# Performance work log

Hardware: AMD Instinct MI355X
Metric: run time of the kernel (lower is better)

The kernel has to match this reference:

```python
import jax, jax.numpy as jnp
import numpy as np

D_MODEL = 256
D_STATE = 32
D_CONV = 8
EXPAND = 4
D_INNER = EXPAND * D_MODEL  # 1024
DT_RANK = (D_MODEL + 15) // 16  # 16
EPS = 1e-5


def setup_inputs() -> dict:
    key = jax.random.key(0)
    ks = jax.random.split(key, 12)
    s = lambda *sh: 1.0 / np.sqrt(sh[-1])
    inp = {
        "x": jax.random.normal(ks[0], (8, 1024, D_MODEL), dtype=jnp.float32),
        "norm_w": jnp.ones((D_MODEL,), jnp.float32),
        "norm_b": jnp.zeros((D_MODEL,), jnp.float32),
        "in_proj_w": jax.random.normal(ks[1], (2 * D_INNER, D_MODEL), jnp.float32) * s(D_MODEL),
        "conv_w": jax.random.normal(ks[2], (D_INNER, 1, D_CONV), jnp.float32) * s(D_CONV),
        "conv_b": jax.random.normal(ks[3], (D_INNER,), jnp.float32) * 0.02,
        "x_proj_w": jax.random.normal(ks[4], (DT_RANK + 2 * D_STATE, D_INNER), jnp.float32) * s(D_INNER),
        "dt_proj_w": jax.random.normal(ks[5], (D_INNER, DT_RANK), jnp.float32) * s(DT_RANK),
        "dt_proj_b": jax.random.uniform(ks[6], (D_INNER,), jnp.float32, -4.0, -1.0),  # dt bias init
        "A_log": jnp.log(jnp.broadcast_to(jnp.arange(1, D_STATE + 1, dtype=jnp.float32), (D_INNER, D_STATE))),
        "D": jnp.ones((D_INNER,), jnp.float32),
        "out_proj_w": jax.random.normal(ks[7], (D_MODEL, D_INNER), jnp.float32) * s(D_INNER),
    }
    return inp


def _mamba_block(x, norm_w, norm_b, in_proj_w, conv_w, conv_b, x_proj_w,
                 dt_proj_w, dt_proj_b, A_log, D, out_proj_w):
    B_, L, _ = x.shape
    residual = x
    # LayerNorm
    mu = jnp.mean(x, -1, keepdims=True)
    var = jnp.mean(jnp.square(x - mu), -1, keepdims=True)
    xn = (x - mu) * jax.lax.rsqrt(var + EPS) * norm_w + norm_b
    # in_proj -> (u, z), each (B, L, D_INNER)
    xz = jnp.einsum("bld,ed->ble", xn, in_proj_w)
    u, z = jnp.split(xz, 2, axis=-1)
    # causal depthwise conv1d along L
    u_ncl = u.transpose(0, 2, 1)  # (B, D_INNER, L)
    u_conv = jax.lax.conv_general_dilated(
        u_ncl, conv_w, window_strides=(1,), padding=[(D_CONV - 1, 0)],
        feature_group_count=D_INNER, dimension_numbers=("NCH", "OIH", "NCH"))
    u_conv = u_conv + conv_b[None, :, None]
    u = jax.nn.silu(u_conv.transpose(0, 2, 1))  # (B, L, D_INNER)
    # x_proj -> dt, Bmat, Cmat
    x_dbl = jnp.einsum("bld,ed->ble", u, x_proj_w)
    dt, Bm, Cm = jnp.split(x_dbl, [DT_RANK, DT_RANK + D_STATE], axis=-1)
    delta = jax.nn.softplus(jnp.einsum("blr,dr->bld", dt, dt_proj_w) + dt_proj_b)
    A = -jnp.exp(A_log)  # (D_INNER, D_STATE)

    # selective scan over L; carry h: (B, D_INNER, D_STATE)
    def step(h, inp):
        d_t, B_t, C_t, u_t = inp  # (B,Di), (B,N), (B,N), (B,Di)
        dA = jnp.exp(d_t[..., None] * A)                       # (B,Di,N)
        dBu = d_t[..., None] * B_t[:, None, :] * u_t[..., None]
        h = dA * h + dBu
        y = jnp.einsum("bdn,bn->bd", h, C_t)
        return h, y

    xs = (delta.transpose(1, 0, 2), Bm.transpose(1, 0, 2),
          Cm.transpose(1, 0, 2), u.transpose(1, 0, 2))
    h0 = jnp.zeros((B_, D_INNER, D_STATE), delta.dtype)
    _, ys = jax.lax.scan(step, h0, xs)
    y = ys.transpose(1, 0, 2)  # (B, L, D_INNER)
    y = y + u * D
    y = y * jax.nn.silu(z)
    out = jnp.einsum("ble,de->bld", y, out_proj_w)
    # dropout is identity in eval mode
    return out + residual


def reference(x, norm_w, norm_b, in_proj_w, conv_w, conv_b, x_proj_w,
              dt_proj_w, dt_proj_b, A_log, D, out_proj_w):
    return _mamba_block(x, norm_w, norm_b, in_proj_w, conv_w, conv_b, x_proj_w,
                        dt_proj_w, dt_proj_b, A_log, D, out_proj_w)
```

## Files before the change

kernel.cpp:

```cpp
#include <hip/hip_runtime.h>
#include <hip/hip_bf16.h>
#include <math.h>


typedef float          f32x4 __attribute__((ext_vector_type(4)));
typedef float          f32x2 __attribute__((ext_vector_type(2)));
typedef short          s16x8 __attribute__((ext_vector_type(8)));
typedef unsigned short u16;
typedef u16            u16x4 __attribute__((ext_vector_type(4)));

#define DEV __device__ __forceinline__

DEV float bf2f(u16 u) { unsigned int i = ((unsigned int)u) << 16; return __builtin_bit_cast(float, i); }
DEV u16 f2bf(float f) {
  unsigned int x = __builtin_bit_cast(unsigned int, f);
  unsigned int r = (x + 0x7FFFu + ((x >> 16) & 1u)) >> 16;
  return (u16)r;
}
DEV float sigmoidf_(float x) { return 1.0f / (1.0f + __expf(-x)); }

__global__ void k_cast(const float* __restrict__ s, u16* __restrict__ d, int n) {
  int i = blockIdx.x * 256 + threadIdx.x;
  if (i < n) d[i] = f2bf(s[i]);
}
__global__ void k_pad_dtw(const float* __restrict__ s, u16* __restrict__ d) {
  int i = blockIdx.x * 256 + threadIdx.x;
  int row = i >> 5, k = i & 31;
  d[i] = (k < 16) ? f2bf(s[row * 16 + k]) : (u16)0;
}

__global__ __launch_bounds__(256) void k_ln(const float* __restrict__ x,
    const float* __restrict__ w, const float* __restrict__ b, u16* __restrict__ xn) {
  int row  = blockIdx.x * 4 + (threadIdx.x >> 6);
  int lane = threadIdx.x & 63;
  const float* xr = x + (size_t)row * 256 + lane * 4;
  f32x4 v = *(const f32x4*)xr;
  float s  = v[0] + v[1] + v[2] + v[3];
  float s2 = v[0]*v[0] + v[1]*v[1] + v[2]*v[2] + v[3]*v[3];
  for (int off = 32; off; off >>= 1) { s += __shfl_xor(s, off); s2 += __shfl_xor(s2, off); }
  float mu  = s * (1.0f / 256.0f);
  float inv = rsqrtf(s2 * (1.0f / 256.0f) - mu * mu + 1e-5f);
  int c = lane * 4;
  u16x4 o;
  #pragma unroll
  for (int t = 0; t < 4; ++t) o[t] = f2bf((v[t] - mu) * inv * w[c + t] + b[c + t]);
  *(u16x4*)(xn + (size_t)row * 256 + c) = o;
}

template<int WAVES_M, int WAVES_N, int WM, int WN, int EPI>
__global__ __launch_bounds__(WAVES_M * WAVES_N * 64)
void k_gemm(const u16* __restrict__ A, const u16* __restrict__ Bw,
            float* __restrict__ Cf, u16* __restrict__ Cb,
            const float* __restrict__ extra,
            int lda, int ldb, int ldc, int Ktiles, int Kact) {
  constexpr int BM = WAVES_M * WM * 16;
  constexpr int BN = WAVES_N * WN * 16;
  constexpr int BK = 32, LDP = BK + 8;
  constexpr int THREADS = WAVES_M * WAVES_N * 64;
  __shared__ u16 As[BM][LDP];
  __shared__ u16 Bs[BN][LDP];
  const int tid = threadIdx.x;
  const int m0 = blockIdx.x * BM, n0 = blockIdx.y * BN;
  const int w = tid >> 6, lane = tid & 63;
  const int wm = w / WAVES_N, wn = w % WAVES_N;
  const int r = lane & 15, kg = lane >> 4, ks = kg * 8;

  f32x4 acc[WM][WN] = {};

  for (int kt = 0; kt < Ktiles; ++kt) {
    const int k0 = kt * BK;
    for (int ci = tid; ci < BM * 4; ci += THREADS) {
      int row = ci >> 2, k8 = (ci & 3) * 8;
      s16x8 vv = {0, 0, 0, 0, 0, 0, 0, 0};
      if (k0 + k8 < Kact)
        vv = *(const s16x8*)(A + (size_t)(m0 + row) * lda + k0 + k8);
      *(s16x8*)(&As[row][k8]) = vv;
    }
    for (int ci = tid; ci < BN * 4; ci += THREADS) {
      int row = ci >> 2, k8 = (ci & 3) * 8;
      *(s16x8*)(&Bs[row][k8]) = *(const s16x8*)(Bw + (size_t)(n0 + row) * ldb + k0 + k8);
    }
    __syncthreads();
    s16x8 af[WM], bfr[WN];
    #pragma unroll
    for (int i = 0; i < WM; ++i) af[i]  = *(const s16x8*)(&As[wm * WM * 16 + i * 16 + r][ks]);
    #pragma unroll
    for (int j = 0; j < WN; ++j) bfr[j] = *(const s16x8*)(&Bs[wn * WN * 16 + j * 16 + r][ks]);
    #pragma unroll
    for (int i = 0; i < WM; ++i)
      #pragma unroll
      for (int j = 0; j < WN; ++j)
        acc[i][j] = __builtin_amdgcn_mfma_f32_16x16x32_bf16(af[i], bfr[j], acc[i][j], 0, 0, 0);
    __syncthreads();
  }

  if constexpr (EPI == 5) {
    #pragma unroll
    for (int i = 0; i < WM; ++i)
      #pragma unroll
      for (int j = 0; j < WN; ++j) {
        int m_base = m0 + wm * WM * 16 + i * 16 + kg * 4;
        int d_ = n0 + wn * WN * 16 + j * 16 + r;
        f32x4 dlt, gv;
        #pragma unroll
        for (int q = 0; q < 4; ++q) {
          float v = acc[i][j][q] + extra[d_];
          v = (v > 20.0f) ? v : log1pf(expf(v));
          dlt[q] = v;
          gv[q] = v * bf2f(Cb[(size_t)(m_base + q) * 1024 + d_]);
        }
        size_t tidx = (size_t)d_ * 8192 + m_base;
        *(f32x4*)(Cf + tidx) = dlt;
        *(f32x4*)(Cf + 8388608 + tidx) = gv;
      }
  } else {
    #pragma unroll
    for (int i = 0; i < WM; ++i)
      #pragma unroll
      for (int j = 0; j < WN; ++j)
        #pragma unroll
        for (int q = 0; q < 4; ++q) {
          int gr = m0 + wm * WM * 16 + i * 16 + kg * 4 + q;
          int gc = n0 + wn * WN * 16 + j * 16 + r;
          float v = acc[i][j][q];
          size_t idx = (size_t)gr * ldc + gc;
          if constexpr (EPI == 1) Cb[idx] = f2bf(v);
          else if constexpr (EPI == 3) Cf[idx] = v + extra[idx];
          else if constexpr (EPI == 4) {
            int b_ = gr >> 10, l_ = gr & 1023;
            if (gc < 16)      Cb[(size_t)gr * 16 + gc] = f2bf(v);
            else if (gc < 48) Cf[(size_t)b_ * 65536 + (size_t)l_ * 64 + (gc - 16) * 2] = v;
            else              Cf[(size_t)b_ * 65536 + (size_t)l_ * 64 + (gc - 48) * 2 + 1] = v;
          }
        }
  }
}

__global__ __launch_bounds__(256) void k_conv(const u16* __restrict__ xz,
    const float* __restrict__ cw, const float* __restrict__ cb, u16* __restrict__ u) {
  int d = (blockIdx.x & 3) * 256 + threadIdx.x;
  int m = blockIdx.x >> 2;
  int l = m & 1023;
  const f32x4* wv = (const f32x4*)(cw + (size_t)d * 8);
  f32x4 w0 = wv[0], w1 = wv[1];
  float acc = cb[d];
  #pragma unroll
  for (int j = 0; j < 8; ++j) {
    int li = l - 7 + j;
    float wj = (j < 4) ? w0[j] : w1[j - 4];
    if (li >= 0) acc = fmaf(bf2f(xz[(size_t)(m - 7 + j) * 2048 + d]), wj, acc);
  }
  u[(size_t)m * 1024 + d] = f2bf(acc * sigmoidf_(acc));
}

template<int C, int RM, bool BC>
DEV float dpp_add(float x) {
  int s = __builtin_amdgcn_update_dpp(0, __builtin_bit_cast(int, x), C, RM, 0xf, BC);
  return x + __builtin_bit_cast(float, s);
}

__global__ __launch_bounds__(256) void k_scan(const float* __restrict__ deltaT,
    const float* __restrict__ gT, const float* __restrict__ BC,
    const float* __restrict__ A_log, float* __restrict__ y) {
  constexpr int CH = 64, NC = 1024 / CH;
  __shared__ float sBC[2][CH][64];
  const int b = blockIdx.x >> 7, dblk = blockIdx.x & 127;
  const int d0 = dblk * 8;
  const int t = threadIdx.x;
  const int n = t & 31, dloc = t >> 5;
  const int d = d0 + dloc;
  const float Adn = -__expf(A_log[d * 32 + n]) * 1.442695040888963f;
  const int stRow = t >> 5;
  const int stCol = (t & 31) * 2;
  const float* src = BC + (size_t)b * 65536;

  f32x2 rr[8];
  auto load_chunk = [&](int c) {
    const int l0 = c * CH;
    #pragma unroll
    for (int i = 0; i < 8; ++i)
      rr[i] = *(const f32x2*)(src + (size_t)(l0 + stRow + 8 * i) * 64 + stCol);
  };
  auto write_chunk = [&](int buf) {
    #pragma unroll
    for (int i = 0; i < 8; ++i)
      *(f32x2*)(&sBC[buf][stRow + 8 * i][stCol]) = rr[i];
  };

  load_chunk(0);
  write_chunk(0);
  __syncthreads();

  const float* dTp = deltaT + (size_t)d * 8192 + (size_t)b * 1024;
  const float* gTp = gT     + (size_t)d * 8192 + (size_t)b * 1024;
  float* yp = y + ((size_t)b * 1024) * 1024 + d;
  float h = 0.0f;
  const bool writer = ((t & 31) == 31);
  f32x4 dv4 = *(const f32x4*)(dTp);
  f32x4 g4  = *(const f32x4*)(gTp);
  for (int c = 0; c < NC; ++c) {
    const int cur = c & 1;
    if (c + 1 < NC) load_chunk(c + 1);
    const int l0c = c * CH;
    for (int l4 = 0; l4 < CH; l4 += 4) {
      const int lg = l0c + l4;
      f32x4 dv4n = dv4, g4n = g4;
      if (lg + 4 < 1024) {
        dv4n = *(const f32x4*)(dTp + lg + 4);
        g4n  = *(const f32x4*)(gTp + lg + 4);
      }
      #pragma unroll
      for (int j = 0; j < 4; ++j) {
        f32x2 bc = *(const f32x2*)(&sBC[cur][l4 + j][2 * n]);
        float dA = exp2f(dv4[j] * Adn);
        h = fmaf(dA, h, g4[j] * bc[0]);
        float p = h * bc[1];
        p = dpp_add<0x111, 0xf, true >(p);
        p = dpp_add<0x112, 0xf, true >(p);
        p = dpp_add<0x114, 0xf, true >(p);
        p = dpp_add<0x118, 0xf, true >(p);
        p = dpp_add<0x142, 0xa, false>(p);
        if (writer) yp[(size_t)(lg + j) * 1024] = p;
      }
      dv4 = dv4n; g4 = g4n;
    }
    if (c + 1 < NC) {
      write_chunk(cur ^ 1);
      __syncthreads();
    }
  }
}

__global__ __launch_bounds__(256) void k_yfinal(const float* __restrict__ y,
    const u16* __restrict__ u, const u16* __restrict__ xz,
    const float* __restrict__ Dv, u16* __restrict__ yb) {
  int i = blockIdx.x * 256 + threadIdx.x;
  int m = i >> 8, d = (i & 255) * 4;
  f32x4 yv = *(const f32x4*)(y + (size_t)m * 1024 + d);
  u16x4 uv = *(const u16x4*)(u + (size_t)m * 1024 + d);
  u16x4 zv = *(const u16x4*)(xz + (size_t)m * 2048 + 1024 + d);
  f32x4 Dw = *(const f32x4*)(Dv + d);
  u16x4 o;
  #pragma unroll
  for (int t = 0; t < 4; ++t) {
    float z = bf2f(zv[t]);
    float val = (yv[t] + bf2f(uv[t]) * Dw[t]) * (z * sigmoidf_(z));
    o[t] = f2bf(val);
  }
  *(u16x4*)(yb + (size_t)m * 1024 + d) = o;
}

extern "C" void kernel_launch(void* const* d_in, const int* in_sizes, int n_in,
                              void* d_out, int out_size, void* d_ws, size_t ws_size,
                              hipStream_t stream) {
  const float* x    = (const float*)d_in[0];
  const float* nw   = (const float*)d_in[1];
  const float* nb   = (const float*)d_in[2];
  const float* win  = (const float*)d_in[3];
  const float* cw   = (const float*)d_in[4];
  const float* cb   = (const float*)d_in[5];
  const float* wxp  = (const float*)d_in[6];
  const float* wdt  = (const float*)d_in[7];
  const float* dtb  = (const float*)d_in[8];
  const float* alog = (const float*)d_in[9];
  const float* Dv   = (const float*)d_in[10];
  const float* wout = (const float*)d_in[11];
  float* out = (float*)d_out;

  char* p = (char*)d_ws;
  auto alloc = [&](size_t bytes) { char* r = p; p += (bytes + 255) & ~(size_t)255; return r; };
  u16*   xn    = (u16*)  alloc((size_t)8192 * 256 * 2);
  u16*   winb  = (u16*)  alloc((size_t)2048 * 256 * 2);
  u16*   wxpb  = (u16*)  alloc((size_t)80 * 1024 * 2);
  u16*   wdtb  = (u16*)  alloc((size_t)1024 * 32 * 2);
  u16*   woutb = (u16*)  alloc((size_t)256 * 1024 * 2);
  u16*   xz    = (u16*)  alloc((size_t)8192 * 2048 * 2);
  u16*   ub    = (u16*)  alloc((size_t)8192 * 1024 * 2);
  u16*   dtbf  = (u16*)  alloc((size_t)8192 * 16 * 2);
  float* bcbuf = (float*)alloc((size_t)8 * 1024 * 64 * 4);
  float* dTgT  = (float*)alloc((size_t)2 * 8192 * 1024 * 4);
  float* ysc   = (float*)alloc((size_t)8192 * 1024 * 4);
  u16*   ybf   = (u16*)  alloc((size_t)8192 * 1024 * 2);

  k_cast<<<2048, 256, 0, stream>>>(win, winb, 2048 * 256);
  k_cast<<<320, 256, 0, stream>>>(wxp, wxpb, 80 * 1024);
  k_pad_dtw<<<128, 256, 0, stream>>>(wdt, wdtb);
  k_cast<<<1024, 256, 0, stream>>>(wout, woutb, 256 * 1024);

  k_ln<<<2048, 256, 0, stream>>>(x, nw, nb, xn);
  k_gemm<2, 2, 4, 4, 1><<<dim3(64, 16), 256, 0, stream>>>(xn, winb, nullptr, xz, nullptr,
                                                          256, 256, 2048, 8, 256);
  k_conv<<<32768, 256, 0, stream>>>(xz, cw, cb, ub);
  k_gemm<2, 1, 1, 5, 4><<<dim3(256, 1), 128, 0, stream>>>(ub, wxpb, bcbuf, dtbf, nullptr,
                                                          1024, 1024, 80, 32, 1024);
  k_gemm<2, 2, 4, 4, 5><<<dim3(64, 8), 256, 0, stream>>>(dtbf, wdtb, dTgT, ub, dtb,
                                                         16, 32, 8192, 1, 16);
  k_scan<<<1024, 256, 0, stream>>>(dTgT, dTgT + 8388608, bcbuf, alog, ysc);
  k_yfinal<<<8192, 256, 0, stream>>>(ysc, ub, xz, Dv, ybf);
  k_gemm<2, 2, 2, 2, 3><<<dim3(128, 4), 256, 0, stream>>>(ybf, woutb, out, nullptr, x,
                                                          1024, 1024, 256, 32, 1024);
}
```

Baseline: 449.2 us.

## Scan two SSM states per thread with 16 channels per block

The selective scan now gives each thread two state elements instead of one, so a 16-lane group covers one channel and a block handles 16 channels. The grid shrinks to 512 blocks. The x_proj epilogue interleaves B and C in pairs so each thread reads one float4 from LDS. This cuts the cross-lane reduction from five DPP steps to four and shares the shared-memory B/C chunk across more channels, at the cost of fewer blocks and less parallelism on the sequential scan.

Result: faster. 413.2 us (-8.0%).

```diff
diff --git a/kernel.cpp b/kernel.cpp
--- a/kernel.cpp
+++ b/kernel.cpp
@@ -129,8 +129,13 @@
           else if constexpr (EPI == 4) {
             int b_ = gr >> 10, l_ = gr & 1023;
             if (gc < 16)      Cb[(size_t)gr * 16 + gc] = f2bf(v);
-            else if (gc < 48) Cf[(size_t)b_ * 65536 + (size_t)l_ * 64 + (gc - 16) * 2] = v;
-            else              Cf[(size_t)b_ * 65536 + (size_t)l_ * 64 + (gc - 48) * 2 + 1] = v;
+            else if (gc < 48) {
+              int n_ = gc - 16;
+              Cf[(size_t)b_ * 65536 + (size_t)l_ * 64 + 4 * (n_ >> 1) + (n_ & 1)] = v;
+            } else {
+              int n_ = gc - 48;
+              Cf[(size_t)b_ * 65536 + (size_t)l_ * 64 + 4 * (n_ >> 1) + 2 + (n_ & 1)] = v;
+            }
           }
         }
   }
@@ -164,12 +169,14 @@
     const float* __restrict__ A_log, float* __restrict__ y) {
   constexpr int CH = 64, NC = 1024 / CH;
   __shared__ float sBC[2][CH][64];
-  const int b = blockIdx.x >> 7, dblk = blockIdx.x & 127;
-  const int d0 = dblk * 8;
+  const int b = blockIdx.x >> 6, dblk = blockIdx.x & 63;
   const int t = threadIdx.x;
-  const int n = t & 31, dloc = t >> 5;
-  const int d = d0 + dloc;
-  const float Adn = -__expf(A_log[d * 32 + n]) * 1.442695040888963f;
+  const int k16 = t & 15;
+  const int dloc = t >> 4;
+  const int d = dblk * 16 + dloc;
+  const float LOG2E = 1.442695040888963f;
+  const float Adn0 = -__expf(A_log[d * 32 + 2 * k16])     * LOG2E;
+  const float Adn1 = -__expf(A_log[d * 32 + 2 * k16 + 1]) * LOG2E;
   const int stRow = t >> 5;
   const int stCol = (t & 31) * 2;
   const float* src = BC + (size_t)b * 65536;
@@ -194,8 +201,8 @@
   const float* dTp = deltaT + (size_t)d * 8192 + (size_t)b * 1024;
   const float* gTp = gT     + (size_t)d * 8192 + (size_t)b * 1024;
   float* yp = y + ((size_t)b * 1024) * 1024 + d;
-  float h = 0.0f;
-  const bool writer = ((t & 31) == 31);
+  float h0 = 0.0f, h1 = 0.0f;
+  const bool writer = (k16 == 15);
   f32x4 dv4 = *(const f32x4*)(dTp);
   f32x4 g4  = *(const f32x4*)(gTp);
   for (int c = 0; c < NC; ++c) {
@@ -211,15 +218,16 @@
       }
       #pragma unroll
       for (int j = 0; j < 4; ++j) {
-        f32x2 bc = *(const f32x2*)(&sBC[cur][l4 + j][2 * n]);
-        float dA = exp2f(dv4[j] * Adn);
-        h = fmaf(dA, h, g4[j] * bc[0]);
-        float p = h * bc[1];
-        p = dpp_add<0x111, 0xf, true >(p);
-        p = dpp_add<0x112, 0xf, true >(p);
-        p = dpp_add<0x114, 0xf, true >(p);
-        p = dpp_add<0x118, 0xf, true >(p);
-        p = dpp_add<0x142, 0xa, false>(p);
+        f32x4 bc = *(const f32x4*)(&sBC[cur][l4 + j][4 * k16]);
+        float dA0 = exp2f(dv4[j] * Adn0);
+        float dA1 = exp2f(dv4[j] * Adn1);
+        h0 = fmaf(dA0, h0, g4[j] * bc[0]);
+        h1 = fmaf(dA1, h1, g4[j] * bc[1]);
+        float p = fmaf(h1, bc[3], h0 * bc[2]);
+        p = dpp_add<0x111, 0xf, true>(p);
+        p = dpp_add<0x112, 0xf, true>(p);
+        p = dpp_add<0x114, 0xf, true>(p);
+        p = dpp_add<0x118, 0xf, true>(p);
         if (writer) yp[(size_t)(lg + j) * 1024] = p;
       }
       dv4 = dv4n; g4 = g4n;
@@ -295,7 +303,7 @@
                                                           1024, 1024, 80, 32, 1024);
   k_gemm<2, 2, 4, 4, 5><<<dim3(64, 8), 256, 0, stream>>>(dtbf, wdtb, dTgT, ub, dtb,
                                                          16, 32, 8192, 1, 16);
-  k_scan<<<1024, 256, 0, stream>>>(dTgT, dTgT + 8388608, bcbuf, alog, ysc);
+  k_scan<<<512, 256, 0, stream>>>(dTgT, dTgT + 8388608, bcbuf, alog, ysc);
   k_yfinal<<<8192, 256, 0, stream>>>(ysc, ub, xz, Dv, ybf);
   k_gemm<2, 2, 2, 2, 3><<<dim3(128, 4), 256, 0, stream>>>(ybf, woutb, out, nullptr, x,
                                                           1024, 1024, 256, 32, 1024);
```
